# Performance work log

Measured on AMD Instinct MI355X. Metric: run time of the kernel, lower is better.

Reference implementation:

```python
import jax, jax.numpy as jnp
import numpy as np

N = 50000      # nodes
E = 800000     # edges (avg degree 16)
F_IN = 128
HID = 64
NCLS = 40
K = 2          # num_stacks
T = 2          # num_layers (shared weights)


def setup_inputs() -> dict:
    key = jax.random.key(0)
    ks = jax.random.split(key, 10)
    s = 0.05
    return {
        "x": jax.random.normal(ks[0], (N, F_IN), dtype=jnp.float32),
        "edge_index": jax.random.randint(ks[1], (2, E), 0, N),
        "w1_init": jax.random.normal(ks[2], (K, F_IN, HID), dtype=jnp.float32) * s,
        "w1": jax.random.normal(ks[3], (K, HID, HID), dtype=jnp.float32) * s,
        "v1": jax.random.normal(ks[4], (K, F_IN, HID), dtype=jnp.float32) * s,
        "b1": jax.random.normal(ks[5], (K, HID), dtype=jnp.float32) * s,
        "w2_init": jax.random.normal(ks[6], (K, HID, NCLS), dtype=jnp.float32) * s,
        "w2": jax.random.normal(ks[7], (K, NCLS, NCLS), dtype=jnp.float32) * s,
        "v2": jax.random.normal(ks[8], (K, HID, NCLS), dtype=jnp.float32) * s,
        "b2": jax.random.normal(ks[9], (K, NCLS), dtype=jnp.float32) * s,
    }


def _gcn_norm(src, dst, n):
    # PyG gcn_norm with add_self_loops=False: deg over destination, sym norm
    deg = jax.ops.segment_sum(jnp.ones_like(dst, dtype=jnp.float32), dst, num_segments=n)
    dinv = jnp.where(deg > 0, 1.0 / jnp.sqrt(deg), 0.0)
    return dinv[src] * dinv[dst]  # [E]


def _arma_conv(x, src, dst, norm, n, w_init, w, v, b, act):
    # x: [N, Fin]; w_init: [K, Fin, Fout]; w: [K, Fout, Fout]; v: [K, Fin, Fout]; b: [K, Fout]
    root = jnp.einsum('nf,kfg->kng', x, v)  # [K, N, Fout], dropout=0 -> identity
    out = None
    for t in range(T):
        if t == 0:
            h = jnp.einsum('nf,kfg->kng', x, w_init)
        else:
            h = jnp.einsum('knf,kfg->kng', out, w)
        # sparse neighbor aggregation: out[i] = sum_{(j->i)} norm_e * h[j]
        agg = jax.vmap(
            lambda hk: jax.ops.segment_sum(hk[src] * norm[:, None], dst, num_segments=n)
        )(h)  # [K, N, Fout]
        out = act(agg + root + b[:, None, :])
    return out.mean(axis=0)  # mean over stacks -> [N, Fout]


def reference(x, edge_index, w1_init, w1, v1, b1, w2_init, w2, v2, b2):
    src, dst = edge_index[0], edge_index[1]
    norm = _gcn_norm(src, dst, N)
    h = _arma_conv(x, src, dst, norm, N, w1_init, w1, v1, b1, jax.nn.relu)
    h = jax.nn.relu(h)  # wrapper ReLU; dropout is identity in eval
    o = _arma_conv(h, src, dst, norm, N, w2_init, w2, v2, b2, lambda z: z)
    return jax.nn.log_softmax(o, axis=1)
```

## Files before the change

kernel.cpp:

```cpp
#include <hip/hip_runtime.h>
#include <hip/hip_bf16.h>
#include <math.h>

#define N_NODES 50000
#define F_IN 128
#define HID 64
#define NCLS 40
#define K_STACKS 2
#define SCAN_TILE 1024
#define NBLK_CNT 256

typedef __attribute__((ext_vector_type(8))) short short8;
typedef __attribute__((ext_vector_type(4))) float floatx4;
typedef __attribute__((ext_vector_type(2))) float floatx2;

__device__ __forceinline__ unsigned int f32_to_bf16_bits(float f) {
    unsigned int u = __float_as_uint(f);
    return (u + 0x7fffu + ((u >> 16) & 1u)) >> 16;
}
__device__ __forceinline__ unsigned int pack_bf16x2(float a, float b) {
    return f32_to_bf16_bits(a) | (f32_to_bf16_bits(b) << 16);
}
__device__ __forceinline__ unsigned char f32_to_fp8(float v) {
    int pk = __builtin_amdgcn_cvt_pk_fp8_f32(v, v, 0, false);
    return (unsigned char)(pk & 0xff);
}


__global__ __launch_bounds__(256) void count_kernel(const int* __restrict__ dst,
                                                    int* __restrict__ counts,
                                                    int* __restrict__ tileSums, int E) {
    __shared__ int hist[256];
    __shared__ int ts[64];
    int blk = blockIdx.x, t = threadIdx.x;
    hist[t] = 0;
    if (t < 64) ts[t] = 0;
    __syncthreads();
    int chunk = (E + NBLK_CNT - 1) / NBLK_CNT;
    int s = blk * chunk, e = min(E, s + chunk);
    for (int i = s + t; i < e; i += 256) atomicAdd(&hist[dst[i] >> 8], 1);
    __syncthreads();
    counts[t * NBLK_CNT + blk] = hist[t];
    atomicAdd(&ts[t >> 2], hist[t]);
    __syncthreads();
    if (t < 64) atomicAdd(&tileSums[t], ts[t]);
}

__global__ __launch_bounds__(256) void scan_phase3_excl(const int* __restrict__ in,
                                                        const int* __restrict__ tileSums,
                                                        int* __restrict__ out, int n) {
    __shared__ int lds[256];
    __shared__ int tsum[64];
    int b = blockIdx.x, t = threadIdx.x;
    if (t < 64) tsum[t] = tileSums[t];
    int base = b * SCAN_TILE + t * 4;
    int e[4];
    int s = 0;
#pragma unroll
    for (int i = 0; i < 4; ++i) {
        e[i] = (base + i < n) ? in[base + i] : 0;
        s += e[i];
    }
    lds[t] = s;
    __syncthreads();
    int v = s;
    for (int off = 1; off < 256; off <<= 1) {
        int add = (t >= off) ? lds[t - off] : 0;
        __syncthreads();
        v += add;
        lds[t] = v;
        __syncthreads();
    }
    int toff = 0;
    for (int i = 0; i < b; ++i) toff += tsum[i];
    int run = (t == 0 ? 0 : lds[t - 1]) + toff;
#pragma unroll
    for (int i = 0; i < 4; ++i) {
        if (base + i < n) {
            out[base + i] = run;
            run += e[i];
        }
    }
}

__global__ __launch_bounds__(256) void bucket_scatter_kernel(const int* __restrict__ src,
                                                             const int* __restrict__ dst,
                                                             const int* __restrict__ scanned,
                                                             unsigned int* __restrict__ pairs,
                                                             int E) {
    __shared__ int cur[256];
    int blk = blockIdx.x, t = threadIdx.x;
    cur[t] = scanned[t * NBLK_CNT + blk];
    __syncthreads();
    int chunk = (E + NBLK_CNT - 1) / NBLK_CNT;
    int s0 = blk * chunk, e0 = min(E, s0 + chunk);
    for (int i = s0 + t; i < e0; i += 256) {
        int d = dst[i];
        int pos = atomicAdd(&cur[d >> 8], 1);
        pairs[pos] = (unsigned int)src[i] | ((unsigned int)(d & 255) << 16);
    }
}

__global__ __launch_bounds__(256) void csr_build_kernel(const unsigned int* __restrict__ pairs,
                                                        const int* __restrict__ scanned,
                                                        int* __restrict__ row_ptr,
                                                        float* __restrict__ dinv,
                                                        int* __restrict__ col, int N, int E) {
    __shared__ int degl[256], lds[256], curl[256], sb[2];
    int b = blockIdx.x, t = threadIdx.x;
    if (t == 0) {
        sb[0] = scanned[b * NBLK_CNT];
        sb[1] = (b + 1 < 256) ? scanned[(b + 1) * NBLK_CNT] : E;
    }
    degl[t] = 0;
    __syncthreads();
    int bstart = sb[0], bend = sb[1];
    for (int e = bstart + t; e < bend; e += 256) {
        atomicAdd(&degl[(pairs[e] >> 16) & 255], 1);
    }
    __syncthreads();
    int d = degl[t];
    lds[t] = d;
    __syncthreads();
    int v = d;
    for (int off = 1; off < 256; off <<= 1) {
        int add = (t >= off) ? lds[t - off] : 0;
        __syncthreads();
        v += add;
        lds[t] = v;
        __syncthreads();
    }
    int excl = v - d;
    int node = b * 256 + t;
    if (node <= N) row_ptr[node] = bstart + excl;
    if (node < N) dinv[node] = (d > 0) ? (1.0f / sqrtf((float)d)) : 0.0f;
    curl[t] = excl;
    __syncthreads();
    for (int e = bstart + t; e < bend; e += 256) {
        unsigned int p = pairs[e];
        int ln = (p >> 16) & 255;
        int pos = atomicAdd(&curl[ln], 1);
        col[bstart + pos] = (int)(p & 0xffffu);
    }
}

__device__ __forceinline__ void wt_one(const float* __restrict__ in,
                                       unsigned short* __restrict__ out, int li, int C, int F,
                                       int CP) {
    int k = li / (F * CP);
    int r = li - k * F * CP;
    int f = r / CP;
    int c = r - f * CP;
    out[li] = (c < C) ? (unsigned short)f32_to_bf16_bits(in[((size_t)k * C + c) * F + f]) : 0;
}

__global__ void wt_all_kernel(const float* v1, const float* w1i, const float* w1,
                              const float* v2, const float* w2i, const float* w2,
                              unsigned short* v1t, unsigned short* w1it, unsigned short* w1t,
                              unsigned short* v2t, unsigned short* w2it, unsigned short* w2t) {
    int i = blockIdx.x * blockDim.x + threadIdx.x;
    if (i < 16384) wt_one(v1, v1t, i, 128, 64, 128);
    else if (i < 32768) wt_one(w1i, w1it, i - 16384, 128, 64, 128);
    else if (i < 40960) wt_one(w1, w1t, i - 32768, 64, 64, 64);
    else if (i < 46080) wt_one(v2, v2t, i - 40960, 64, 40, 64);
    else if (i < 51200) wt_one(w2i, w2it, i - 46080, 64, 40, 64);
    else if (i < 56320) wt_one(w2, w2t, i - 51200, 40, 40, 64);
}

template <int CINP>
__device__ __forceinline__ void stage_A(const void* A, unsigned short* At, size_t abase,
                                        int n0, int t, int N, int CREAL, int a_bf16,
                                        int stride) {
    constexpr int CP8 = CINP / 8;
    constexpr int MS = CP8 - 1;
    constexpr int SH = (CP8 == 16) ? 4 : 3;
    for (int i = t; i < 64 * CP8; i += stride) {
        int n = i >> SH;
        int c = i & MS;
        uint4 w = make_uint4(0u, 0u, 0u, 0u);
        int gn = n0 + n;
        if (gn < N && c * 8 < CREAL) {
            if (a_bf16) {
                w = *(const uint4*)((const unsigned short*)A + abase + (size_t)gn * CREAL + c * 8);
            } else {
                const float* srcp = (const float*)A + abase + (size_t)gn * CREAL + c * 8;
                float4 f0 = *(const float4*)(srcp);
                float4 f1 = *(const float4*)(srcp + 4);
                w.x = pack_bf16x2(f0.x, f0.y);
                w.y = pack_bf16x2(f0.z, f0.w);
                w.z = pack_bf16x2(f1.x, f1.y);
                w.w = pack_bf16x2(f1.z, f1.w);
            }
        }
        *(uint4*)(At + n * CINP + ((c ^ (n & MS)) << 3)) = w;
    }
}

template <int CINP>
__device__ __forceinline__ void stage_B(const unsigned short* Bk, unsigned short* Bs, int t,
                                        int COUT, int stride) {
    constexpr int CP8 = CINP / 8;
    constexpr int MS = CP8 - 1;
    constexpr int SH = (CP8 == 16) ? 4 : 3;
    for (int i = t; i < COUT * CP8; i += stride) {
        int f = i >> SH;
        int c = i & MS;
        uint4 w = *(const uint4*)(Bk + f * CINP + c * 8);
        *(uint4*)(Bs + f * CINP + ((c ^ (f & MS)) << 3)) = w;
    }
}

template <int CINP>
__global__ __launch_bounds__(256) void gemm2_mfma(
    const void* __restrict__ A, const unsigned short* __restrict__ Bt1,
    const unsigned short* __restrict__ Bt2, unsigned short* __restrict__ out1,
    unsigned char* __restrict__ out2, const float* __restrict__ scale, int N, int COUT,
    int CREAL, int a_bf16) {
    constexpr int MS = CINP / 8 - 1;
    __shared__ __align__(16) unsigned short At[64 * CINP];
    __shared__ __align__(16) unsigned short Bs1[64 * CINP];
    __shared__ __align__(16) unsigned short Bs2[64 * CINP];

    const int k = blockIdx.y;
    const int n0 = blockIdx.x * 64;
    const int t = threadIdx.x;
    stage_A<CINP>(A, At, (size_t)0, n0, t, N, CREAL, a_bf16, 256);
    stage_B<CINP>(Bt1 + (size_t)k * COUT * CINP, Bs1, t, COUT, 256);
    stage_B<CINP>(Bt2 + (size_t)k * COUT * CINP, Bs2, t, COUT, 256);
    __syncthreads();

    const int lane = t & 63;
    const int wv = t >> 6;
    const int quad = lane >> 4;
    const int li = lane & 15;
    const int m0 = wv * 16;

    floatx4 acc1[4] = {{0.f, 0.f, 0.f, 0.f}, {0.f, 0.f, 0.f, 0.f},
                       {0.f, 0.f, 0.f, 0.f}, {0.f, 0.f, 0.f, 0.f}};
    floatx4 acc2[4] = {{0.f, 0.f, 0.f, 0.f}, {0.f, 0.f, 0.f, 0.f},
                       {0.f, 0.f, 0.f, 0.f}, {0.f, 0.f, 0.f, 0.f}};
    const int am = (m0 + li) & MS;
#pragma unroll
    for (int kc = 0; kc < CINP / 32; ++kc) {
        int cc = kc * 4 + quad;
        short8 a = *(const short8*)(At + (m0 + li) * CINP + ((cc ^ am) << 3));
#pragma unroll
        for (int nt = 0; nt < 4; ++nt) {
            if (nt * 16 < COUT) {
                int f = nt * 16 + li;
                int bo = f * CINP + ((cc ^ (f & MS)) << 3);
                short8 b1 = *(const short8*)(Bs1 + bo);
                short8 b2 = *(const short8*)(Bs2 + bo);
                acc1[nt] = __builtin_amdgcn_mfma_f32_16x16x32_bf16(a, b1, acc1[nt], 0, 0, 0);
                acc2[nt] = __builtin_amdgcn_mfma_f32_16x16x32_bf16(a, b2, acc2[nt], 0, 0, 0);
            }
        }
    }

    float sc[4];
#pragma unroll
    for (int r = 0; r < 4; ++r) {
        int node = n0 + m0 + quad * 4 + r;
        sc[r] = (node < N) ? scale[node] : 1.f;
    }
#pragma unroll
    for (int nt = 0; nt < 4; ++nt) {
        if (nt * 16 >= COUT) continue;
        int f = nt * 16 + li;
        if (f >= COUT) continue;
#pragma unroll
        for (int r = 0; r < 4; ++r) {
            int node = n0 + m0 + quad * 4 + r;
            if (node < N) {
                out1[((size_t)k * N + node) * COUT + f] =
                    (unsigned short)f32_to_bf16_bits(acc1[nt][r]);
                out2[(size_t)node * 2 * COUT + (size_t)k * COUT + f] =
                    f32_to_fp8(acc2[nt][r] * sc[r]);
            }
        }
    }
}

template <int F, int COUT, int FMODE>
__global__ __launch_bounds__(512) void agg_gemm_kernel(
    const unsigned char* __restrict__ h8, const int* __restrict__ row_ptr,
    const int* __restrict__ col, const float* __restrict__ dinv,
    const unsigned short* __restrict__ rootb, const float* __restrict__ bias,
    const unsigned short* __restrict__ Bt1, const unsigned short* __restrict__ Bt2,
    unsigned short* __restrict__ rootOut, unsigned char* __restrict__ tblOut, int N) {
    constexpr int NA = (FMODE == 1) ? 1 : 2;
    constexpr int NB = (FMODE == 1) ? 4 : 2;
    constexpr int BT = COUT * 64;
    constexpr int NT = (COUT + 15) / 16;
    constexpr int FH = F / 8;
    constexpr int ROWB = 2 * F;
    __shared__ __align__(16) unsigned short At[NA * 64 * 64];
    __shared__ __align__(16) unsigned short Bs[NB * BT];
    __shared__ int rp[65];
    __shared__ float dvl[64];

    const int n0 = blockIdx.x * 64;
    const int t = threadIdx.x;

    stage_B<64>(Bt1, Bs, t, COUT, 512);
    stage_B<64>(Bt1 + (size_t)COUT * 64, Bs + BT, t, COUT, 512);
    if constexpr (FMODE == 1) {
        stage_B<64>(Bt2, Bs + 2 * BT, t, COUT, 512);
        stage_B<64>(Bt2 + (size_t)COUT * 64, Bs + 3 * BT, t, COUT, 512);
    }
    if (t < 65) rp[t] = row_ptr[min(n0 + t, N)];
    if (t < 64) dvl[t] = (n0 + t < N) ? dinv[n0 + t] : 0.f;
    __syncthreads();

    const int lane = t & 63;
    const int wv = t >> 6;
    const int half = lane >> 5;
    const int l32 = lane & 31;
    const int sub = l32 >> 4;
    const int fq = l32 & 15;
    const int kk = fq >> 3;
    const int fqq = fq & 7;
    const int fqc = (fqq < FH) ? fqq : (FH - 1);
    const int foff = kk * F + fqc * 8;

#pragma unroll 1
    for (int p = 0; p < 4; ++p) {
        const int nl = wv * 8 + p * 2 + half;
        const int node = n0 + nl;
        const bool valid = node < N;
        const int e0 = rp[nl];
        const int deg = rp[nl + 1] - e0;
        const float dv = dvl[nl];
        float acc[8] = {};
        for (int w0 = 0; w0 < deg; w0 += 32) {
            int mye = w0 + l32;
            int c = (mye < deg) ? col[e0 + mye] : 0;
            int nch = min(deg - w0, 32);
            for (int base = 0; base < nch; base += 16) {
                uint2 v[8];
                float wj[8];
#pragma unroll
                for (int u = 0; u < 8; ++u) {
                    int j = base + u * 2 + sub;
                    int cj = __shfl(c, (half << 5) | (j & 31));
                    bool ok = (j < nch);
                    wj[u] = ok ? 1.f : 0.f;
                    int cs = ok ? cj : 0;
                    v[u] = *(const uint2*)(h8 + (size_t)cs * ROWB + foff);
                }
#pragma unroll
                for (int u = 0; u < 8; ++u) {
                    floatx2 f0 = __builtin_amdgcn_cvt_pk_f32_fp8(v[u].x, false);
                    floatx2 f1 = __builtin_amdgcn_cvt_pk_f32_fp8(v[u].x, true);
                    floatx2 f2 = __builtin_amdgcn_cvt_pk_f32_fp8(v[u].y, false);
                    floatx2 f3 = __builtin_amdgcn_cvt_pk_f32_fp8(v[u].y, true);
                    acc[0] += wj[u] * f0.x;
                    acc[1] += wj[u] * f0.y;
                    acc[2] += wj[u] * f1.x;
                    acc[3] += wj[u] * f1.y;
                    acc[4] += wj[u] * f2.x;
                    acc[5] += wj[u] * f2.y;
                    acc[6] += wj[u] * f3.x;
                    acc[7] += wj[u] * f3.y;
                }
            }
        }
#pragma unroll
        for (int i = 0; i < 8; ++i) acc[i] += __shfl_xor(acc[i], 16);

        size_t oc = ((size_t)kk * N + (valid ? node : 0)) * F + fqc * 8;
        uint4 rv = *(const uint4*)(rootb + oc);
        const float* bp = bias + kk * F + fqc * 8;
        float4 b0 = *(const float4*)(bp);
        float4 b1_ = *(const float4*)(bp + 4);
        const unsigned int ru[4] = {rv.x, rv.y, rv.z, rv.w};
        float res[8];
#pragma unroll
        for (int q = 0; q < 4; ++q) {
            float rlo = __uint_as_float(ru[q] << 16);
            float rhi = __uint_as_float(ru[q] & 0xffff0000u);
            float blo = (q < 2) ? ((q == 0) ? b0.x : b0.z) : ((q == 2) ? b1_.x : b1_.z);
            float bhi = (q < 2) ? ((q == 0) ? b0.y : b0.w) : ((q == 2) ? b1_.y : b1_.w);
            res[2 * q] = acc[2 * q] * dv + rlo + blo;
            res[2 * q + 1] = acc[2 * q + 1] * dv + rhi + bhi;
        }
        if constexpr (FMODE != 2) {
#pragma unroll
            for (int i = 0; i < 8; ++i) res[i] = fmaxf(res[i], 0.f);
        }
        if constexpr (FMODE == 1) {
            float mres[8];
#pragma unroll
            for (int i = 0; i < 8; ++i) mres[i] = 0.5f * (res[i] + __shfl_xor(res[i], 8));
            if (sub == 0 && kk == 0) {
                uint4 w;
                w.x = pack_bf16x2(mres[0], mres[1]);
                w.y = pack_bf16x2(mres[2], mres[3]);
                w.z = pack_bf16x2(mres[4], mres[5]);
                w.w = pack_bf16x2(mres[6], mres[7]);
                *(uint4*)(At + nl * 64 + ((fqq ^ (nl & 7)) << 3)) = w;
            }
        } else {
            if (sub == 0) {
                uint4 w = make_uint4(0u, 0u, 0u, 0u);
                if (fqq < FH) {
                    w.x = pack_bf16x2(res[0], res[1]);
                    w.y = pack_bf16x2(res[2], res[3]);
                    w.z = pack_bf16x2(res[4], res[5]);
                    w.w = pack_bf16x2(res[6], res[7]);
                }
                *(uint4*)(At + kk * 4096 + nl * 64 + ((fqq ^ (nl & 7)) << 3)) = w;
            }
        }
    }
    __syncthreads();

    const int quad = lane >> 4;
    const int li = lane & 15;
    const int kSel = wv >> 2;
    const int m0 = (wv & 3) * 16;
    const int am = (m0 + li) & 7;

    if constexpr (FMODE == 1) {
        floatx4 aR[NT] = {};
        floatx4 aT[NT] = {};
#pragma unroll
        for (int kc = 0; kc < 2; ++kc) {
            int cc = kc * 4 + quad;
            short8 a = *(const short8*)(At + (m0 + li) * 64 + ((cc ^ am) << 3));
#pragma unroll
            for (int nt = 0; nt < NT; ++nt) {
                int f = nt * 16 + li;
                int fc = (COUT & 15) ? ((f < COUT) ? f : (COUT - 1)) : f;
                int bo = fc * 64 + ((cc ^ (fc & 7)) << 3);
                short8 bR = *(const short8*)(Bs + kSel * BT + bo);
                short8 bT = *(const short8*)(Bs + (2 + kSel) * BT + bo);
                aR[nt] = __builtin_amdgcn_mfma_f32_16x16x32_bf16(a, bR, aR[nt], 0, 0, 0);
                aT[nt] = __builtin_amdgcn_mfma_f32_16x16x32_bf16(a, bT, aT[nt], 0, 0, 0);
            }
        }
#pragma unroll
        for (int nt = 0; nt < NT; ++nt) {
            int f = nt * 16 + li;
            if (f >= COUT) continue;
#pragma unroll
            for (int r = 0; r < 4; ++r) {
                int nl2 = m0 + quad * 4 + r;
                int node = n0 + nl2;
                if (node < N) {
                    rootOut[((size_t)kSel * N + node) * COUT + f] =
                        (unsigned short)f32_to_bf16_bits(aR[nt][r]);
                    tblOut[(size_t)node * 2 * COUT + (size_t)kSel * COUT + f] =
                        f32_to_fp8(aT[nt][r] * dvl[nl2]);
                }
            }
        }
    } else {
        floatx4 ac[NT] = {};
#pragma unroll
        for (int kc = 0; kc < 2; ++kc) {
            int cc = kc * 4 + quad;
            short8 a = *(const short8*)(At + kSel * 4096 + (m0 + li) * 64 + ((cc ^ am) << 3));
#pragma unroll
            for (int nt = 0; nt < NT; ++nt) {
                int f = nt * 16 + li;
                int fc = (COUT & 15) ? ((f < COUT) ? f : (COUT - 1)) : f;
                int bo = fc * 64 + ((cc ^ (fc & 7)) << 3);
                short8 b = *(const short8*)(Bs + kSel * BT + bo);
                ac[nt] = __builtin_amdgcn_mfma_f32_16x16x32_bf16(a, b, ac[nt], 0, 0, 0);
            }
        }
#pragma unroll
        for (int nt = 0; nt < NT; ++nt) {
            int f = nt * 16 + li;
            if (f >= COUT) continue;
#pragma unroll
            for (int r = 0; r < 4; ++r) {
                int nl2 = m0 + quad * 4 + r;
                int node = n0 + nl2;
                if (node < N)
                    tblOut[(size_t)node * 2 * COUT + (size_t)kSel * COUT + f] =
                        f32_to_fp8(ac[nt][r] * dvl[nl2]);
            }
        }
    }
}

template <int F>
__global__ __launch_bounds__(256) void agg_kernel(
    const unsigned char* __restrict__ h8, const int* __restrict__ row_ptr,
    const int* __restrict__ col, const float* __restrict__ dinv,
    const unsigned short* __restrict__ rootb, const float* __restrict__ bias,
    void* __restrict__ out, int N, int do_relu, int mode) {
    constexpr int FH = F / 8;
    constexpr int ROWB = 2 * F;
    int wid = (blockIdx.x * blockDim.x + threadIdx.x) >> 6;
    int lane = threadIdx.x & 63;
    int half = lane >> 5;
    int l32 = lane & 31;
    int node = wid * 2 + half;
    bool valid = node < N;
    int e0 = 0, deg = 0;
    float dv = 0.f;
    if (valid) {
        e0 = row_ptr[node];
        deg = row_ptr[node + 1] - e0;
        dv = dinv[node];
    }
    const int sub = l32 >> 4;
    const int fq = l32 & 15;
    const int kk = fq >> 3;
    const int fqq = fq & 7;
    const int fqc = (fqq < FH) ? fqq : (FH - 1);
    const int foff = kk * F + fqc * 8;

    float acc[8] = {};
    for (int w0 = 0; w0 < deg; w0 += 32) {
        int mye = w0 + l32;
        int c = (mye < deg) ? col[e0 + mye] : 0;
        int nch = min(deg - w0, 32);
        for (int base = 0; base < nch; base += 16) {
            uint2 v[8];
            float wj[8];
#pragma unroll
            for (int u = 0; u < 8; ++u) {
                int j = base + u * 2 + sub;
                int cj = __shfl(c, (half << 5) | (j & 31));
                bool ok = (j < nch);
                wj[u] = ok ? 1.f : 0.f;
                int cs = ok ? cj : 0;
                v[u] = *(const uint2*)(h8 + (size_t)cs * ROWB + foff);
            }
#pragma unroll
            for (int u = 0; u < 8; ++u) {
                floatx2 f0 = __builtin_amdgcn_cvt_pk_f32_fp8(v[u].x, false);
                floatx2 f1 = __builtin_amdgcn_cvt_pk_f32_fp8(v[u].x, true);
                floatx2 f2 = __builtin_amdgcn_cvt_pk_f32_fp8(v[u].y, false);
                floatx2 f3 = __builtin_amdgcn_cvt_pk_f32_fp8(v[u].y, true);
                acc[0] += wj[u] * f0.x;
                acc[1] += wj[u] * f0.y;
                acc[2] += wj[u] * f1.x;
                acc[3] += wj[u] * f1.y;
                acc[4] += wj[u] * f2.x;
                acc[5] += wj[u] * f2.y;
                acc[6] += wj[u] * f3.x;
                acc[7] += wj[u] * f3.y;
            }
        }
    }
#pragma unroll
    for (int i = 0; i < 8; ++i) acc[i] += __shfl_xor(acc[i], 16);

    size_t oc = ((size_t)kk * N + (valid ? node : 0)) * F + fqc * 8;
    uint4 rv = *(const uint4*)(rootb + oc);
    const float* bp = bias + kk * F + fqc * 8;
    float4 b0 = *(const float4*)(bp);
    float4 b1 = *(const float4*)(bp + 4);
    const unsigned int ru[4] = {rv.x, rv.y, rv.z, rv.w};
    float res[8];
#pragma unroll
    for (int q = 0; q < 4; ++q) {
        float rlo = __uint_as_float(ru[q] << 16);
        float rhi = __uint_as_float(ru[q] & 0xffff0000u);
        float blo = (q < 2) ? ((q == 0) ? b0.x : b0.z) : ((q == 2) ? b1.x : b1.z);
        float bhi = (q < 2) ? ((q == 0) ? b0.y : b0.w) : ((q == 2) ? b1.y : b1.w);
        res[2 * q] = acc[2 * q] * dv + rlo + blo;
        res[2 * q + 1] = acc[2 * q + 1] * dv + rhi + bhi;
    }
    if (do_relu) {
#pragma unroll
        for (int i = 0; i < 8; ++i) res[i] = fmaxf(res[i], 0.f);
    }
    if (mode == 0) {
        if (sub == 0 && fqq < FH && valid) {
            size_t o = ((size_t)kk * N + node) * F + fqq * 8;
            uint4 w;
            w.x = pack_bf16x2(res[0], res[1]);
            w.y = pack_bf16x2(res[2], res[3]);
            w.z = pack_bf16x2(res[4], res[5]);
            w.w = pack_bf16x2(res[6], res[7]);
            *(uint4*)((unsigned short*)out + o) = w;
        }
    } else {
        float mres[8];
#pragma unroll
        for (int i = 0; i < 8; ++i) mres[i] = 0.5f * (res[i] + __shfl_xor(res[i], 8));
        if (mode == 1) {
            if (sub == 0 && kk == 0 && fqq < FH && valid) {
                size_t o = (size_t)node * F + fqq * 8;
                *(float4*)((float*)out + o) = make_float4(mres[0], mres[1], mres[2], mres[3]);
                *(float4*)((float*)out + o + 4) = make_float4(mres[4], mres[5], mres[6], mres[7]);
            }
        } else {
            bool act = (fqq < FH);
            float lm = -INFINITY;
            if (act) {
#pragma unroll
                for (int i = 0; i < 8; ++i) lm = fmaxf(lm, mres[i]);
            }
#pragma unroll
            for (int m = 1; m < 8; m <<= 1) lm = fmaxf(lm, __shfl_xor(lm, m));
            float ls = 0.f;
            if (act) {
#pragma unroll
                for (int i = 0; i < 8; ++i) ls += expf(mres[i] - lm);
            }
#pragma unroll
            for (int m = 1; m < 8; m <<= 1) ls += __shfl_xor(ls, m);
            float lg = lm + logf(ls);
            if (sub == 0 && kk == 0 && act && valid) {
                size_t o = (size_t)node * F + fqq * 8;
                *(float4*)((float*)out + o) =
                    make_float4(mres[0] - lg, mres[1] - lg, mres[2] - lg, mres[3] - lg);
                *(float4*)((float*)out + o + 4) =
                    make_float4(mres[4] - lg, mres[5] - lg, mres[6] - lg, mres[7] - lg);
            }
        }
    }
}


static inline size_t align256(size_t x) { return (x + 255) & ~(size_t)255; }

extern "C" void kernel_launch(void* const* d_in, const int* in_sizes, int n_in,
                              void* d_out, int out_size, void* d_ws, size_t ws_size,
                              hipStream_t stream) {
    const float* x = (const float*)d_in[0];
    const int* ei = (const int*)d_in[1];
    const float* w1_init = (const float*)d_in[2];
    const float* w1 = (const float*)d_in[3];
    const float* v1 = (const float*)d_in[4];
    const float* b1 = (const float*)d_in[5];
    const float* w2_init = (const float*)d_in[6];
    const float* w2 = (const float*)d_in[7];
    const float* v2 = (const float*)d_in[8];
    const float* b2 = (const float*)d_in[9];

    const int N = in_sizes[0] / F_IN;
    const int E = in_sizes[1] / 2;
    const int* src = ei;
    const int* dst = ei + E;

    char* p = (char*)d_ws;
    auto take = [&](size_t bytes) {
        char* r = p;
        p += align256(bytes);
        return r;
    };
    float* dinv = (float*)take((size_t)N * 4);
    int* row_ptr = (int*)take((size_t)(N + 1) * 4);
    int* tileSums = (int*)take(256 * 4);
    int* counts = (int*)take((size_t)256 * NBLK_CNT * 4);
    int* scanned = (int*)take((size_t)256 * NBLK_CNT * 4);
    unsigned int* pairs = (unsigned int*)take((size_t)E * 4);
    int* col = (int*)take((size_t)E * 4);
    unsigned short* v1t = (unsigned short*)take((size_t)2 * 64 * 128 * 2);
    unsigned short* w1it = (unsigned short*)take((size_t)2 * 64 * 128 * 2);
    unsigned short* w1t = (unsigned short*)take((size_t)2 * 64 * 64 * 2);
    unsigned short* v2t = (unsigned short*)take((size_t)2 * 40 * 64 * 2);
    unsigned short* w2it = (unsigned short*)take((size_t)2 * 40 * 64 * 2);
    unsigned short* w2t = (unsigned short*)take((size_t)2 * 40 * 64 * 2);
    unsigned short* rootb = (unsigned short*)take((size_t)K_STACKS * N * HID * 2);
    unsigned short* root2 = (unsigned short*)take((size_t)K_STACKS * N * NCLS * 2);
    unsigned char* tblA = (unsigned char*)take((size_t)K_STACKS * N * HID);
    unsigned char* tblB = (unsigned char*)take((size_t)K_STACKS * N * HID);

    const int TB = 256;
    const int nCnt = 256 * NBLK_CNT;
    const int nScanBlocks = nCnt / SCAN_TILE;
    const int nBuckets = (N + 255) / 256;
    const int ntiles = (N + 63) / 64;

    hipMemsetAsync(tileSums, 0, 256, stream);
    count_kernel<<<NBLK_CNT, 256, 0, stream>>>(dst, counts, tileSums, E);
    scan_phase3_excl<<<nScanBlocks, 256, 0, stream>>>(counts, tileSums, scanned, nCnt);
    bucket_scatter_kernel<<<NBLK_CNT, 256, 0, stream>>>(src, dst, scanned, pairs, E);
    csr_build_kernel<<<nBuckets, 256, 0, stream>>>(pairs, scanned, row_ptr, dinv, col, N, E);

    wt_all_kernel<<<(56320 + TB - 1) / TB, TB, 0, stream>>>(v1, w1_init, w1, v2, w2_init, w2,
                                                            v1t, w1it, w1t, v2t, w2it, w2t);

    dim3 ggrid(ntiles, K_STACKS);
    const int agg_blocks = ((N + 1) / 2 + 3) / 4;

    gemm2_mfma<128><<<ggrid, 256, 0, stream>>>(x, v1t, w1it, rootb, tblA, dinv, N, HID, 128, 0);
    agg_gemm_kernel<HID, HID, 0><<<ntiles, 512, 0, stream>>>(
        tblA, row_ptr, col, dinv, rootb, b1, w1t, nullptr, nullptr, tblB, N);

    agg_gemm_kernel<HID, NCLS, 1><<<ntiles, 512, 0, stream>>>(
        tblB, row_ptr, col, dinv, rootb, b1, v2t, w2it, root2, tblA, N);

    agg_gemm_kernel<NCLS, NCLS, 2><<<ntiles, 512, 0, stream>>>(
        tblA, row_ptr, col, dinv, root2, b2, w2t, nullptr, nullptr, tblB, N);

    agg_kernel<NCLS><<<agg_blocks, 256, 0, stream>>>(tblB, row_ptr, col, dinv, root2, b2,
                                                     (float*)d_out, N, 0, 2);
}
```

Before: 274.4 us.

## Merge both stacks into one 512-thread GEMM block and read weights directly

The first dense GEMM now launches one 512-thread block per 64-node tile covering both stacks, with waves 4-7 handling the second stack. The x tile is loaded from memory and staged into LDS once instead of twice. Weight fragments are read straight from global memory (cached) instead of being staged through LDS, which cuts LDS usage and staging time. The cost is uncoalesced-ish global loads for B in the inner loop, and the kernel is now specialised to fixed sizes.

```diff
diff --git a/kernel.cpp b/kernel.cpp
--- a/kernel.cpp
+++ b/kernel.cpp
@@ -210,50 +210,45 @@
     }
 }
 
-template <int CINP>
-__global__ __launch_bounds__(256) void gemm2_mfma(
-    const void* __restrict__ A, const unsigned short* __restrict__ Bt1,
+__global__ __launch_bounds__(512) void gemm2k(
+    const float* __restrict__ A, const unsigned short* __restrict__ Bt1,
     const unsigned short* __restrict__ Bt2, unsigned short* __restrict__ out1,
-    unsigned char* __restrict__ out2, const float* __restrict__ scale, int N, int COUT,
-    int CREAL, int a_bf16) {
-    constexpr int MS = CINP / 8 - 1;
+    unsigned char* __restrict__ out2, const float* __restrict__ scale, int N) {
+    constexpr int CINP = 128;
+    constexpr int MS = 15;
     __shared__ __align__(16) unsigned short At[64 * CINP];
-    __shared__ __align__(16) unsigned short Bs1[64 * CINP];
-    __shared__ __align__(16) unsigned short Bs2[64 * CINP];
-
-    const int k = blockIdx.y;
+
     const int n0 = blockIdx.x * 64;
     const int t = threadIdx.x;
-    stage_A<CINP>(A, At, (size_t)0, n0, t, N, CREAL, a_bf16, 256);
-    stage_B<CINP>(Bt1 + (size_t)k * COUT * CINP, Bs1, t, COUT, 256);
-    stage_B<CINP>(Bt2 + (size_t)k * COUT * CINP, Bs2, t, COUT, 256);
+    stage_A<CINP>(A, At, (size_t)0, n0, t, N, CINP, 0, 512);
     __syncthreads();
 
     const int lane = t & 63;
     const int wv = t >> 6;
+    const int kSel = wv >> 2;
+    const int m0 = (wv & 3) * 16;
     const int quad = lane >> 4;
     const int li = lane & 15;
-    const int m0 = wv * 16;
+    const int am = (m0 + li) & MS;
+    const unsigned short* B1k = Bt1 + (size_t)kSel * 64 * CINP;
+    const unsigned short* B2k = Bt2 + (size_t)kSel * 64 * CINP;
 
     floatx4 acc1[4] = {{0.f, 0.f, 0.f, 0.f}, {0.f, 0.f, 0.f, 0.f},
                        {0.f, 0.f, 0.f, 0.f}, {0.f, 0.f, 0.f, 0.f}};
     floatx4 acc2[4] = {{0.f, 0.f, 0.f, 0.f}, {0.f, 0.f, 0.f, 0.f},
                        {0.f, 0.f, 0.f, 0.f}, {0.f, 0.f, 0.f, 0.f}};
-    const int am = (m0 + li) & MS;
-#pragma unroll
-    for (int kc = 0; kc < CINP / 32; ++kc) {
+#pragma unroll
+    for (int kc = 0; kc < 4; ++kc) {
         int cc = kc * 4 + quad;
         short8 a = *(const short8*)(At + (m0 + li) * CINP + ((cc ^ am) << 3));
 #pragma unroll
         for (int nt = 0; nt < 4; ++nt) {
-            if (nt * 16 < COUT) {
-                int f = nt * 16 + li;
-                int bo = f * CINP + ((cc ^ (f & MS)) << 3);
-                short8 b1 = *(const short8*)(Bs1 + bo);
-                short8 b2 = *(const short8*)(Bs2 + bo);
-                acc1[nt] = __builtin_amdgcn_mfma_f32_16x16x32_bf16(a, b1, acc1[nt], 0, 0, 0);
-                acc2[nt] = __builtin_amdgcn_mfma_f32_16x16x32_bf16(a, b2, acc2[nt], 0, 0, 0);
-            }
+            int f = nt * 16 + li;
+            size_t bo = (size_t)f * CINP + cc * 8;
+            short8 b1 = *(const short8*)(B1k + bo);
+            short8 b2 = *(const short8*)(B2k + bo);
+            acc1[nt] = __builtin_amdgcn_mfma_f32_16x16x32_bf16(a, b1, acc1[nt], 0, 0, 0);
+            acc2[nt] = __builtin_amdgcn_mfma_f32_16x16x32_bf16(a, b2, acc2[nt], 0, 0, 0);
         }
     }
 
@@ -265,16 +260,14 @@
     }
 #pragma unroll
     for (int nt = 0; nt < 4; ++nt) {
-        if (nt * 16 >= COUT) continue;
         int f = nt * 16 + li;
-        if (f >= COUT) continue;
 #pragma unroll
         for (int r = 0; r < 4; ++r) {
             int node = n0 + m0 + quad * 4 + r;
             if (node < N) {
-                out1[((size_t)k * N + node) * COUT + f] =
+                out1[((size_t)kSel * N + node) * 64 + f] =
                     (unsigned short)f32_to_bf16_bits(acc1[nt][r]);
-                out2[(size_t)node * 2 * COUT + (size_t)k * COUT + f] =
+                out2[(size_t)node * 128 + (size_t)kSel * 64 + f] =
                     f32_to_fp8(acc2[nt][r] * sc[r]);
             }
         }
@@ -680,10 +673,9 @@
     wt_all_kernel<<<(56320 + TB - 1) / TB, TB, 0, stream>>>(v1, w1_init, w1, v2, w2_init, w2,
                                                             v1t, w1it, w1t, v2t, w2it, w2t);
 
-    dim3 ggrid(ntiles, K_STACKS);
     const int agg_blocks = ((N + 1) / 2 + 3) / 4;
 
-    gemm2_mfma<128><<<ggrid, 256, 0, stream>>>(x, v1t, w1it, rootb, tblA, dinv, N, HID, 128, 0);
+    gemm2k<<<ntiles, 512, 0, stream>>>(x, v1t, w1it, rootb, tblA, dinv, N);
     agg_gemm_kernel<HID, HID, 0><<<ntiles, 512, 0, stream>>>(
         tblA, row_ptr, col, dinv, rootb, b1, w1t, nullptr, nullptr, tblB, N);
 
```

After: 276.0 us (median of 2 runs). No clear change (+0.6%).
